# Kernel tuning notes

Measured on AMD Instinct MI355X. Metric: run time of the kernel, lower is better.

## Reference

```python
import jax, jax.numpy as jnp
import numpy as np

B, N, DIM = 16, 3136, 512
HEADS, AGENT, WINDOW = 8, 49, 14


def setup_inputs() -> dict:
    key = jax.random.key(0)
    ks = jax.random.split(key, 14)
    s = 0.02
    return {
        "x": jax.random.normal(ks[0], (B, N, DIM), jnp.float32),
        "w_qkv": jax.random.normal(ks[1], (3 * DIM, DIM), jnp.float32) * 0.02,
        "w_proj": jax.random.normal(ks[2], (DIM, DIM), jnp.float32) * 0.02,
        "b_proj": jnp.zeros((DIM,), jnp.float32),
        "w_dwc": jax.random.normal(ks[3], (DIM, 1, 3, 3), jnp.float32) * 0.1,
        "b_dwc": jnp.zeros((DIM,), jnp.float32),
        "an_bias": jax.random.normal(ks[4], (HEADS, AGENT, 7, 7), jnp.float32) * s,
        "na_bias": jax.random.normal(ks[5], (HEADS, AGENT, 7, 7), jnp.float32) * s,
        "ah_bias": jax.random.normal(ks[6], (1, HEADS, AGENT, WINDOW, 1), jnp.float32) * s,
        "aw_bias": jax.random.normal(ks[7], (1, HEADS, AGENT, 1, WINDOW), jnp.float32) * s,
        "ha_bias": jax.random.normal(ks[8], (1, HEADS, WINDOW, 1, AGENT), jnp.float32) * s,
        "wa_bias": jax.random.normal(ks[9], (1, HEADS, 1, WINDOW, AGENT), jnp.float32) * s,
        "ca_bias": jax.random.normal(ks[10], (1, HEADS, 1, AGENT), jnp.float32) * s,
    }


def reference(x, w_qkv, w_proj, b_proj, w_dwc, b_dwc, an_bias, na_bias,
              ah_bias, aw_bias, ha_bias, wa_bias, ca_bias):
    b, n, c = x.shape
    h = w = int(np.sqrt(n))            # 56x56, static
    nh, hd = HEADS, c // HEADS
    scale = hd ** -0.5
    ww = WINDOW * WINDOW               # 196

    qkv = x @ w_qkv.T                  # (b, n, 3c)
    q, k, v = jnp.split(qkv, 3, axis=-1)

    # agent tokens: adaptive avg-pool q to (7, 7)  (exact block mean, 56/7=8)
    pool = int(AGENT ** 0.5)
    q_img = q.reshape(b, h, w, c).transpose(0, 3, 1, 2)  # (b, c, h, w)
    pooled = q_img.reshape(b, c, pool, h // pool, pool, w // pool).mean(axis=(3, 5))
    agent = pooled.reshape(b, c, AGENT).transpose(0, 2, 1)  # (b, 49, c)

    qh = q.reshape(b, n, nh, hd).transpose(0, 2, 1, 3)      # (b, H, n, d)
    kh = k.reshape(b, n, nh, hd).transpose(0, 2, 1, 3)
    vh = v.reshape(b, n, nh, hd).transpose(0, 2, 1, 3)
    ah = agent.reshape(b, AGENT, nh, hd).transpose(0, 2, 1, 3)  # (b, H, 49, d)

    # ---- stage 1: agent -> kv attention ----
    pb1 = jax.image.resize(an_bias, (nh, AGENT, WINDOW, WINDOW), 'bilinear')
    pb1 = pb1.reshape(1, nh, AGENT, ww)
    pb2 = (ah_bias + aw_bias).reshape(1, nh, AGENT, ww)
    pb = jnp.broadcast_to(pb1 + pb2, (b, nh, AGENT, ww))
    scores1 = jnp.einsum('bhad,bhnd->bhan', ah * scale, kh)     # (b, H, 49, n)
    pb_up = jax.image.resize(pb, scores1.shape, 'bilinear')     # 196 -> n along last dim
    attn1 = jax.nn.softmax(scores1 + pb_up, axis=-1)
    agent_v = jnp.einsum('bhan,bhnd->bhad', attn1, vh)          # (b, H, 49, d)

    # ---- stage 2: query -> agent attention ----
    ab1 = jax.image.resize(na_bias, (nh, AGENT, WINDOW, WINDOW), 'bilinear')
    ab1 = ab1.reshape(1, nh, AGENT, ww).transpose(0, 1, 3, 2)   # (1, H, 196, 49)
    ab2 = (ha_bias + wa_bias).reshape(1, nh, ww, AGENT)
    ab = jnp.broadcast_to(ab1 + ab2, (b, nh, ww, AGENT))
    ab = jnp.concatenate([jnp.broadcast_to(ca_bias, (b, nh, 1, AGENT)), ab], axis=-2)
    scores2 = jnp.einsum('bhnd,bhad->bhna', qh * scale, ah)     # (b, H, n, 49)
    ab_up = jax.image.resize(ab, scores2.shape, 'bilinear')     # 197 -> n along dim -2
    attn2 = jax.nn.softmax(scores2 + ab_up, axis=-1)
    out = jnp.einsum('bhna,bhad->bhnd', attn2, agent_v)
    out = out.transpose(0, 2, 1, 3).reshape(b, n, c)

    # ---- depthwise-conv residual on v ----
    v_img = vh.transpose(0, 2, 1, 3).reshape(b, h, w, c).transpose(0, 3, 1, 2)
    dwc = jax.lax.conv_general_dilated(
        v_img, w_dwc, (1, 1), 'SAME',
        dimension_numbers=('NCHW', 'OIHW', 'NCHW'), feature_group_count=c)
    dwc = dwc + b_dwc[None, :, None, None]
    out = out + dwc.transpose(0, 2, 3, 1).reshape(b, n, c)

    return out @ w_proj.T + b_proj
```

## Files before the change

### kernel.cpp

```cpp
#include <hip/hip_runtime.h>

typedef unsigned short u16;
typedef unsigned int   u32;
typedef unsigned long long u64;
typedef float  f32x4  __attribute__((ext_vector_type(4)));
typedef __bf16 bf16x8 __attribute__((ext_vector_type(8)));

#define DEV static __device__ __forceinline__

DEV float bf2f(u16 u){ union{float f;u32 i;}v; v.i=((u32)u)<<16; return v.f; }
DEV float bflo(u32 u){ union{float f;u32 i;}v; v.i=u<<16; return v.f; }
DEV float bfhi(u32 u){ union{float f;u32 i;}v; v.i=u&0xffff0000u; return v.f; }
DEV u16   f2bf(float f){ union{float f;u32 i;}v; v.f=f; return (u16)((v.i + 0x7fffu + ((v.i>>16)&1u))>>16); }

DEV void async16(const void* g, void* l){
  __builtin_amdgcn_global_load_lds((const __attribute__((address_space(1))) void*)g,
                                   (__attribute__((address_space(3))) void*)l, 16, 0, 0);
}

__global__ __launch_bounds__(256) void cast_bf16(const float* __restrict__ in,
                                                 u16* __restrict__ out, int n4)
{
  int i = blockIdx.x*256 + threadIdx.x;
  if (i >= n4) return;
  float4 v = ((const float4*)in)[i];
  ushort4 o;
  o.x = f2bf(v.x); o.y = f2bf(v.y); o.z = f2bf(v.z); o.w = f2bf(v.w);
  ((ushort4*)out)[i] = o;
}

__global__ __launch_bounds__(256) void gemm_bt(
    const u16* __restrict__ A, const u16* __restrict__ W, int K, int mode,
    u16* __restrict__ oq, u16* __restrict__ okk, u16* __restrict__ ov,
    float* __restrict__ of, const float* __restrict__ bias)
{
  __shared__ __align__(16) u16 As[8192];
  __shared__ __align__(16) u16 Bs[8192];
  const int tid  = threadIdx.x;
  const int wave = tid >> 6, lane = tid & 63;
  const int wm = wave >> 1, wn = wave & 1;
  const int r16 = lane & 15, q4 = lane >> 4;
  const int xr = r16 & 7;
  const size_t Abase = (size_t)blockIdx.x * 128 * K;
  const size_t Bbase = (size_t)blockIdx.y * 128 * K;

  f32x4 acc[4][4];
  #pragma unroll
  for (int i=0;i<4;i++)
    #pragma unroll
    for (int j=0;j<4;j++) acc[i][j] = (f32x4){0.f,0.f,0.f,0.f};

  for (int k0 = 0; k0 < K; k0 += 64) {
    #pragma unroll
    for (int i=0;i<4;i++){
      int s   = i*256 + tid;
      int row = s >> 3;
      int c   = (s & 7) ^ (row & 7);
      async16(A + Abase + (size_t)row*K + k0 + c*8, (char*)As + (size_t)s*16);
      async16(W + Bbase + (size_t)row*K + k0 + c*8, (char*)Bs + (size_t)s*16);
    }
    __syncthreads();
    #pragma unroll
    for (int ks=0; ks<2; ks++){
      const int xo = ((ks*4 + q4) ^ xr) * 8;
      bf16x8 af[4], bfr[4];
      #pragma unroll
      for (int i=0;i<4;i++) af[i]  = *(const bf16x8*)&As[(wm*64 + i*16 + r16)*64 + xo];
      #pragma unroll
      for (int j=0;j<4;j++) bfr[j] = *(const bf16x8*)&Bs[(wn*64 + j*16 + r16)*64 + xo];
      #pragma unroll
      for (int i=0;i<4;i++)
        #pragma unroll
        for (int j=0;j<4;j++)
          acc[i][j] = __builtin_amdgcn_mfma_f32_16x16x32_bf16(bfr[j], af[i], acc[i][j], 0,0,0);
    }
    __syncthreads();
  }

  const int m0 = blockIdx.x*128 + wm*64;
  const int n0 = blockIdx.y*128 + wn*64;
  if (mode == 0){
    int sel = blockIdx.y >> 2;
    u16* dst = sel==0 ? oq : (sel==1 ? okk : ov);
    #pragma unroll
    for (int i=0;i<4;i++){
      int token = m0 + i*16 + r16;
      #pragma unroll
      for (int j=0;j<4;j++){
        int col = (n0 + j*16 + q4*4) & 511;
        uint2 pk;
        pk.x = (u32)f2bf(acc[i][j][0]) | ((u32)f2bf(acc[i][j][1]) << 16);
        pk.y = (u32)f2bf(acc[i][j][2]) | ((u32)f2bf(acc[i][j][3]) << 16);
        *(uint2*)&dst[(size_t)token*512 + col] = pk;
      }
    }
  } else {
    #pragma unroll
    for (int j=0;j<4;j++){
      int nbase = n0 + j*16 + q4*4;
      float4 b4 = *(const float4*)&bias[nbase];
      #pragma unroll
      for (int i=0;i<4;i++){
        int token = m0 + i*16 + r16;
        float4 o4 = { acc[i][j][0]+b4.x, acc[i][j][1]+b4.y,
                      acc[i][j][2]+b4.z, acc[i][j][3]+b4.w };
        *(float4*)&of[(size_t)token*512 + nbase] = o4;
      }
    }
  }
}

__global__ __launch_bounds__(256) void pool_q(const u16* __restrict__ qb, u16* __restrict__ agentb)
{
  int idx = blockIdx.x*256 + threadIdx.x;
  int c = idx & 511;
  int ba = idx >> 9;
  int a = ba & 63, b = ba >> 6;
  if (a >= 49) { agentb[idx] = 0; return; }
  int ay = a / 7, ax = a % 7;
  const u16* base = qb + (size_t)b*3136*512 + c;
  float acc = 0.f;
  #pragma unroll
  for (int iy=0; iy<8; iy++){
    int rowoff = ((ay*8 + iy)*56 + ax*8) * 512;
    #pragma unroll
    for (int ix=0; ix<8; ix++) acc += bf2f(base[(size_t)rowoff + ix*512]);
  }
  agentb[idx] = f2bf(acc * 0.015625f);
}

DEV void lin1(float c, int S, int& i0, int& i1, float& w){
  if (c <= 0.f){ i0=0; i1=0; w=0.f; }
  else if (c >= (float)(S-1)){ i0=S-1; i1=S-1; w=0.f; }
  else { i0=(int)c; i1=i0+1; w=c-(float)i0; }
}
DEV float bilin7(const float* s, int Y, int X){
  int y0,y1,x0,x1; float wy,wx;
  lin1(0.5f*Y - 0.25f, 7, y0,y1,wy);
  lin1(0.5f*X - 0.25f, 7, x0,x1,wx);
  float v0 = s[y0*7+x0] + wx*(s[y0*7+x1]-s[y0*7+x0]);
  float v1 = s[y1*7+x0] + wx*(s[y1*7+x1]-s[y1*7+x0]);
  return v0 + wy*(v1 - v0);
}
__global__ __launch_bounds__(256) void bias_pre(
    const float* __restrict__ an_bias, const float* __restrict__ na_bias,
    const float* __restrict__ ah_bias, const float* __restrict__ aw_bias,
    const float* __restrict__ ha_bias, const float* __restrict__ wa_bias,
    const float* __restrict__ ca_bias, float* __restrict__ PB, float* __restrict__ AB)
{
  int idx = blockIdx.x*256 + threadIdx.x;
  if (idx < 8*49*196){
    int j = idx % 196; int ha = idx / 196; int a = ha % 49, h = ha / 49;
    int wy = j / 14, wx = j % 14;
    PB[idx] = bilin7(an_bias + (h*49+a)*49, wy, wx)
            + ah_bias[(h*49+a)*14 + wy] + aw_bias[(h*49+a)*14 + wx];
  }
  int idx2 = idx - 8*49*196;
  if (idx2 >= 0 && idx2 < 8*197*49){
    int a = idx2 % 49; int hr = idx2 / 49; int r = hr % 197, h = hr / 197;
    float v;
    if (r == 0) v = ca_bias[h*49 + a];
    else {
      int j = r - 1; int wy = j / 14, wx = j % 14;
      v = bilin7(na_bias + (h*49+a)*49, wy, wx)
        + ha_bias[(h*14+wy)*49 + a] + wa_bias[(h*14+wx)*49 + a];
    }
    AB[idx2] = v;
  }
}

__global__ __launch_bounds__(256) void bias_expand2(
    const float* __restrict__ PB, const float* __restrict__ AB,
    float* __restrict__ PBIT, float* __restrict__ ABI)
{
  int idx = blockIdx.x*256 + threadIdx.x;
  if (idx < 1605632) {
    int a = idx & 63; int t = idx >> 6; int n = t % 3136; int h = t / 3136;
    float val = -1e30f;
    if (a < 49) {
      const float* row = PB + (h*49 + a)*196;
      float c1 = (n + 0.5f)*0.0625f - 0.5f;
      if (c1 <= 0.f) val = row[0];
      else if (c1 >= 195.f) val = row[195];
      else { int j0 = (int)c1; float w = c1 - (float)j0; val = row[j0] + w*(row[j0+1]-row[j0]); }
    }
    PBIT[idx] = val;
  } else {
    int idx2 = idx - 1605632;
    if (idx2 >= 1605632) return;
    int a = idx2 & 63; int t = idx2 >> 6; int n = t % 3136; int h = t / 3136;
    float val = -1e30f;
    if (a < 49) {
      float c2 = (n + 0.5f)*(197.0f/3136.0f) - 0.5f;
      int r0; float w;
      if (c2 <= 0.f) { r0 = 0; w = 0.f; }
      else if (c2 >= 196.f) { r0 = 196; w = 0.f; }
      else { r0 = (int)c2; w = c2 - (float)r0; }
      int r1 = (r0 < 196) ? r0 + 1 : 196;
      float v0 = AB[(h*197 + r0)*49 + a];
      float v1 = AB[(h*197 + r1)*49 + a];
      val = v0 + w*(v1 - v0);
    }
    ABI[idx2] = val;
  }
}

__global__ __launch_bounds__(256) void stage1_mfma(
    const u16* __restrict__ kb, const u16* __restrict__ vb,
    const u16* __restrict__ agentb, const float* __restrict__ PBIT,
    float* __restrict__ pav, float* __restrict__ psum)
{
  int bh = blockIdx.x, chunk = blockIdx.y;
  int b = bh >> 3, h = bh & 7;
  int tid = threadIdx.x, lane = tid & 63, w = tid >> 6;
  int r16 = lane & 15, q4 = lane >> 4;
  __shared__ __align__(16) u16 kld[64*64];
  __shared__ __align__(16) u16 vt[64*68];
  __shared__ __align__(16) u16 scb[64*72];

  int agent = w*16 + r16;
  bf16x8 bah[2];
  {
    const u16* ap = agentb + ((size_t)(b*64 + agent))*512 + h*64 + q4*8;
    bah[0] = *(const bf16x8*)ap;
    bah[1] = *(const bf16x8*)(ap + 32);
  }
  f32x4 Oacc[4];
  #pragma unroll
  for (int nt = 0; nt < 4; nt++) Oacc[nt] = (f32x4){0.f,0.f,0.f,0.f};
  float ssum = 0.f;
  int n0 = chunk * 448;
  const u16* kbase = kb + ((size_t)b*3136)*512 + h*64;
  const u16* vbase = vb + ((size_t)b*3136)*512 + h*64;

  for (int it = 0; it < 7; it++) {
    int nt0 = n0 + it*64;
    __syncthreads();
    #pragma unroll
    for (int i = 0; i < 2; i++) {
      int L = w*128 + i*64 + lane;
      int row = L >> 3, colc = (L & 7) ^ (row & 7);
      async16(kbase + (size_t)(nt0 + row)*512 + colc*8, (char*)kld + (w*128 + i*64)*16);
    }
    uint4 va[2]; int vtok[2], vdc[2];
    #pragma unroll
    for (int i = 0; i < 2; i++) {
      int c = tid + i*256;
      vtok[i] = c >> 3; vdc[i] = (c & 7)*8;
      va[i] = *(const uint4*)(vbase + (size_t)(nt0 + vtok[i])*512 + vdc[i]);
    }
    #pragma unroll
    for (int i = 0; i < 2; i++) {
      u32 uu[4] = {va[i].x, va[i].y, va[i].z, va[i].w};
      #pragma unroll
      for (int e = 0; e < 4; e++) {
        vt[(vdc[i] + 2*e + 0)*68 + vtok[i]] = (u16)(uu[e] & 0xffffu);
        vt[(vdc[i] + 2*e + 1)*68 + vtok[i]] = (u16)(uu[e] >> 16);
      }
    }
    __syncthreads();
    f32x4 S[4];
    #pragma unroll
    for (int mt = 0; mt < 4; mt++) S[mt] = (f32x4){0.f,0.f,0.f,0.f};
    #pragma unroll
    for (int ks = 0; ks < 2; ks++)
      #pragma unroll
      for (int mt = 0; mt < 4; mt++) {
        int row = mt*16 + r16;
        int colc = (ks*4 + q4) ^ (row & 7);
        bf16x8 afr = *(const bf16x8*)&kld[row*64 + colc*8];
        S[mt] = __builtin_amdgcn_mfma_f32_16x16x32_bf16(afr, bah[ks], S[mt], 0,0,0);
      }
    #pragma unroll
    for (int mt = 0; mt < 4; mt++) {
      u64 pk = 0;
      #pragma unroll
      for (int r = 0; r < 4; r++) {
        int tokl = mt*16 + q4*4 + r;
        float bias = PBIT[((size_t)h*3136 + nt0 + tokl)*64 + agent];
        float e = __expf(0.125f*S[mt][r] + bias);
        ssum += e;
        pk |= ((u64)f2bf(e)) << (16*r);
      }
      *(u64*)&scb[agent*72 + mt*16 + q4*4] = pk;
    }
    #pragma unroll
    for (int ks = 0; ks < 2; ks++) {
      bf16x8 ap = *(const bf16x8*)&scb[agent*72 + ks*32 + q4*8];
      #pragma unroll
      for (int nt = 0; nt < 4; nt++) {
        union { bf16x8 v; uint2 u[2]; } bb;
        int dim = nt*16 + r16;
        bb.u[0] = *(const uint2*)&vt[dim*68 + ks*32 + q4*8];
        bb.u[1] = *(const uint2*)&vt[dim*68 + ks*32 + q4*8 + 4];
        Oacc[nt] = __builtin_amdgcn_mfma_f32_16x16x32_bf16(ap, bb.v, Oacc[nt], 0,0,0);
      }
    }
  }
  ssum += __shfl_xor(ssum, 16);
  ssum += __shfl_xor(ssum, 32);
  size_t pb = (size_t)chunk*128 + bh;
  #pragma unroll
  for (int nt = 0; nt < 4; nt++)
    #pragma unroll
    for (int r = 0; r < 4; r++)
      pav[(pb*64 + (w*16 + q4*4 + r))*64 + nt*16 + r16] = Oacc[nt][r];
  if (lane < 16) psum[pb*64 + w*16 + lane] = ssum;
}

__global__ __launch_bounds__(256) void reduce_agv(
    const float* __restrict__ pav, const float* __restrict__ psum, u16* __restrict__ avTg)
{
  int idx = blockIdx.x*256 + threadIdx.x;
  int d = idx & 63, a = (idx >> 6) & 63, bh = idx >> 12;
  float val = 0.f;
  if (a < 49) {
    float acc = 0.f, s = 0.f;
    #pragma unroll
    for (int c = 0; c < 7; c++) {
      acc += pav[(((size_t)c*128 + bh)*64 + a)*64 + d];
      s   += psum[((size_t)c*128 + bh)*64 + a];
    }
    val = acc / s;
  }
  avTg[((size_t)bh*64 + d)*72 + a] = f2bf(val);
}

__global__ __launch_bounds__(256) void stage2_mfma(
    const u16* __restrict__ qb, const u16* __restrict__ agentb,
    const u16* __restrict__ avTg, const float* __restrict__ ABI,
    u16* __restrict__ aout)
{
  int bh = blockIdx.x, chunk = blockIdx.y;
  int b = bh >> 3, h = bh & 7;
  int tid = threadIdx.x, lane = tid & 63, w = tid >> 6;
  int r16 = lane & 15, q4 = lane >> 4;
  __shared__ __align__(16) u16 avs[64*72];
  __shared__ __align__(16) u16 scb2[4*16*72];

  const u16* avsrc = avTg + (size_t)bh*4608;
  #pragma unroll
  for (int rr = 0; rr < 3; rr++) {
    int c = rr*256 + w*64 + lane;
    if (c < 576) async16(avsrc + c*8, (char*)avs + ((size_t)rr*256 + w*64)*16);
  }
  bf16x8 bah[4][2];
  #pragma unroll
  for (int nt = 0; nt < 4; nt++) {
    const u16* ap = agentb + ((size_t)(b*64 + nt*16 + r16))*512 + h*64 + q4*8;
    bah[nt][0] = *(const bf16x8*)ap;
    bah[nt][1] = *(const bf16x8*)(ap + 32);
  }
  __syncthreads();

  u16* scw = scb2 + w*16*72;
  for (int t = 0; t < 7; t++) {
    int tok0 = (chunk*28 + w*7 + t)*16;
    bf16x8 aq[2];
    {
      const u16* qp = qb + ((size_t)b*3136 + tok0 + r16)*512 + h*64 + q4*8;
      aq[0] = *(const bf16x8*)qp;
      aq[1] = *(const bf16x8*)(qp + 32);
    }
    f32x4 S[4];
    #pragma unroll
    for (int nt = 0; nt < 4; nt++) S[nt] = (f32x4){0.f,0.f,0.f,0.f};
    #pragma unroll
    for (int ks = 0; ks < 2; ks++)
      #pragma unroll
      for (int nt = 0; nt < 4; nt++)
        S[nt] = __builtin_amdgcn_mfma_f32_16x16x32_bf16(aq[ks], bah[nt][ks], S[nt], 0,0,0);
    float rs[4] = {0.f,0.f,0.f,0.f};
    #pragma unroll
    for (int nt = 0; nt < 4; nt++)
      #pragma unroll
      for (int r = 0; r < 4; r++) {
        int tokl = q4*4 + r;
        float bias = ABI[((size_t)h*3136 + tok0 + tokl)*64 + nt*16 + r16];
        float e = __expf(0.125f*S[nt][r] + bias);
        rs[r] += e;
        scw[tokl*72 + nt*16 + r16] = f2bf(e);
      }
    #pragma unroll
    for (int m = 1; m <= 8; m <<= 1)
      #pragma unroll
      for (int r = 0; r < 4; r++) rs[r] += __shfl_xor(rs[r], m);
    f32x4 O[4];
    #pragma unroll
    for (int nt = 0; nt < 4; nt++) O[nt] = (f32x4){0.f,0.f,0.f,0.f};
    #pragma unroll
    for (int ks = 0; ks < 2; ks++) {
      bf16x8 ap2 = *(const bf16x8*)&scw[r16*72 + ks*32 + q4*8];
      #pragma unroll
      for (int nt = 0; nt < 4; nt++) {
        bf16x8 bv = *(const bf16x8*)&avs[(nt*16 + r16)*72 + ks*32 + q4*8];
        O[nt] = __builtin_amdgcn_mfma_f32_16x16x32_bf16(ap2, bv, O[nt], 0,0,0);
      }
    }
    float inv[4];
    #pragma unroll
    for (int r = 0; r < 4; r++) inv[r] = 1.0f / rs[r];
    #pragma unroll
    for (int nt = 0; nt < 4; nt++)
      #pragma unroll
      for (int r = 0; r < 4; r++)
        aout[((size_t)b*3136 + tok0 + q4*4 + r)*512 + h*64 + nt*16 + r16] = f2bf(O[nt][r]*inv[r]);
  }
}

__global__ __launch_bounds__(256) void dwc_add2(
    const u16* __restrict__ vb, const float* __restrict__ w_dwc,
    const float* __restrict__ b_dwc, u16* __restrict__ io)
{
  int wave = (blockIdx.x << 2) + (threadIdx.x >> 6);
  int lane = threadIdx.x & 63;
  int c0 = lane * 8;

  float wt[9][8];
  {
    float tmp[72];
    const float4* wp = (const float4*)(w_dwc + c0*9);
    #pragma unroll
    for (int i = 0; i < 18; i++) {
      float4 v4 = wp[i];
      tmp[4*i] = v4.x; tmp[4*i+1] = v4.y; tmp[4*i+2] = v4.z; tmp[4*i+3] = v4.w;
    }
    #pragma unroll
    for (int j = 0; j < 8; j++)
      #pragma unroll
      for (int tp = 0; tp < 9; tp++) wt[tp][j] = tmp[j*9 + tp];
  }
  float bias[8];
  {
    const float4* bp = (const float4*)(b_dwc + c0);
    float4 a4 = bp[0], b4 = bp[1];
    bias[0]=a4.x; bias[1]=a4.y; bias[2]=a4.z; bias[3]=a4.w;
    bias[4]=b4.x; bias[5]=b4.y; bias[6]=b4.z; bias[7]=b4.w;
  }

  int t0 = wave * 16;
  int b = t0 / 3136;
  int n0 = t0 - b*3136;
  const u16* vbase = vb + ((size_t)b*3136)*512 + c0;

  for (int ti = 0; ti < 16; ti++) {
    int n = n0 + ti;
    int y = n / 56, x = n - y*56;
    size_t toff = ((size_t)b*3136 + n)*512 + c0;
    float acc[8];
    {
      uint4 uo = *(const uint4*)(io + toff);
      u32 uu[4] = {uo.x, uo.y, uo.z, uo.w};
      #pragma unroll
      for (int e = 0; e < 4; e++) {
        acc[2*e+0] = bflo(uu[e]) + bias[2*e+0];
        acc[2*e+1] = bfhi(uu[e]) + bias[2*e+1];
      }
    }
    #pragma unroll
    for (int dy = 0; dy < 3; dy++) {
      int yy = y + dy - 1;
      if (yy < 0 || yy > 55) continue;
      #pragma unroll
      for (int dx = 0; dx < 3; dx++) {
        int xx = x + dx - 1;
        if (xx < 0 || xx > 55) continue;
        uint4 uv = *(const uint4*)(vbase + ((size_t)(yy*56 + xx) << 9));
        u32 uu[4] = {uv.x, uv.y, uv.z, uv.w};
        const float* wr = wt[dy*3 + dx];
        #pragma unroll
        for (int e = 0; e < 4; e++) {
          acc[2*e+0] += bflo(uu[e]) * wr[2*e+0];
          acc[2*e+1] += bfhi(uu[e]) * wr[2*e+1];
        }
      }
    }
    uint4 pk;
    pk.x = (u32)f2bf(acc[0]) | ((u32)f2bf(acc[1]) << 16);
    pk.y = (u32)f2bf(acc[2]) | ((u32)f2bf(acc[3]) << 16);
    pk.z = (u32)f2bf(acc[4]) | ((u32)f2bf(acc[5]) << 16);
    pk.w = (u32)f2bf(acc[6]) | ((u32)f2bf(acc[7]) << 16);
    *(uint4*)(io + toff) = pk;
  }
}

extern "C" void kernel_launch(void* const* d_in, const int* in_sizes, int n_in,
                              void* d_out, int out_size, void* d_ws, size_t ws_size,
                              hipStream_t stream)
{
  const float* x       = (const float*)d_in[0];
  const float* w_qkv   = (const float*)d_in[1];
  const float* w_proj  = (const float*)d_in[2];
  const float* b_proj  = (const float*)d_in[3];
  const float* w_dwc   = (const float*)d_in[4];
  const float* b_dwc   = (const float*)d_in[5];
  const float* an_bias = (const float*)d_in[6];
  const float* na_bias = (const float*)d_in[7];
  const float* ah_bias = (const float*)d_in[8];
  const float* aw_bias = (const float*)d_in[9];
  const float* ha_bias = (const float*)d_in[10];
  const float* wa_bias = (const float*)d_in[11];
  const float* ca_bias = (const float*)d_in[12];

  if (ws_size < 210000000u) return;

  char* p = (char*)d_ws;
  u16* regA   = (u16*)p;  p += 51380224;
  u16* qb     = (u16*)p;  p += 51380224;
  u16* kb     = (u16*)p;  p += 51380224;
  u16* vb     = (u16*)p;  p += 51380224;
  u16* wqkvb  = (u16*)p;  p += 1572864;
  u16* wprojb = (u16*)p;  p += 524288;
  u16* agentb = (u16*)p;  p += 1048576;
  float* PB   = (float*)p; p += 307456;
  float* AB   = (float*)p; p += 309248;

  float* PBIT = (float*)((char*)regA);
  float* ABI  = (float*)((char*)regA + 6422528);
  float* pav  = (float*)((char*)regA + 12845056);
  float* psum = (float*)((char*)regA + 27525120);
  u16*   avTg = (u16*)  ((char*)regA + 27754496);
  u16*   aout = kb;

  cast_bf16<<<25088, 256, 0, stream>>>(x, regA, 6422528);
  cast_bf16<<<768,   256, 0, stream>>>(w_qkv, wqkvb, 196608);
  cast_bf16<<<256,   256, 0, stream>>>(w_proj, wprojb, 65536);

  gemm_bt<<<dim3(392,12), 256, 0, stream>>>(regA, wqkvb, 512, 0, qb, kb, vb, nullptr, nullptr);
  pool_q<<<2048, 256, 0, stream>>>(qb, agentb);
  bias_pre<<<602, 256, 0, stream>>>(an_bias, na_bias, ah_bias, aw_bias, ha_bias, wa_bias, ca_bias, PB, AB);
  bias_expand2<<<12544, 256, 0, stream>>>(PB, AB, PBIT, ABI);
  stage1_mfma<<<dim3(128,7), 256, 0, stream>>>(kb, vb, agentb, PBIT, pav, psum);
  reduce_agv<<<2048, 256, 0, stream>>>(pav, psum, avTg);
  stage2_mfma<<<dim3(128,7), 256, 0, stream>>>(qb, agentb, avTg, ABI, aout);
  dwc_add2<<<784, 256, 0, stream>>>(vb, w_dwc, b_dwc, aout);
  gemm_bt<<<dim3(392,4), 256, 0, stream>>>(aout, wprojb, 512, 1, nullptr, nullptr, nullptr,
                                           (float*)d_out, b_proj);
}
```

Baseline: 550.3 us.

## Replace 128x128 GEMM with 256x256 double-buffered pipelined MFMA GEMM

Both projection GEMMs now use 256x256 output tiles computed by 512 threads (8 waves) instead of 128x128 tiles with 4 waves, which doubles operand reuse per LDS load. The new kernel double-buffers LDS and issues async global-to-LDS loads for the next K tiles in the middle of the MFMA phases. It coordinates this with explicit barriers, waitcnt instructions and s_setprio, so memory latency can overlap with compute. The catch is 128 KB of LDS per block, more accumulator registers, and fewer blocks in each grid, which can reduce occupancy and load balance across CUs.

Result: faster. 529.6 us (-3.8%).

```diff
diff --git a/kernel.cpp b/kernel.cpp
--- a/kernel.cpp
+++ b/kernel.cpp
@@ -29,65 +29,128 @@
   ((ushort4*)out)[i] = o;
 }
 
-__global__ __launch_bounds__(256) void gemm_bt(
+__global__ __launch_bounds__(512, 2) void gemm256(
     const u16* __restrict__ A, const u16* __restrict__ W, int K, int mode,
     u16* __restrict__ oq, u16* __restrict__ okk, u16* __restrict__ ov,
     float* __restrict__ of, const float* __restrict__ bias)
 {
-  __shared__ __align__(16) u16 As[8192];
-  __shared__ __align__(16) u16 Bs[8192];
+  __shared__ __align__(16) u16 As[2*16384];
+  __shared__ __align__(16) u16 Bs[2*16384];
   const int tid  = threadIdx.x;
-  const int wave = tid >> 6, lane = tid & 63;
-  const int wm = wave >> 1, wn = wave & 1;
+  const int w = tid >> 6, lane = tid & 63;
+  const int wm = w >> 2, wn = w & 3;
   const int r16 = lane & 15, q4 = lane >> 4;
   const int xr = r16 & 7;
-  const size_t Abase = (size_t)blockIdx.x * 128 * K;
-  const size_t Bbase = (size_t)blockIdx.y * 128 * K;
-
-  f32x4 acc[4][4];
+  const size_t Abase = (size_t)blockIdx.x * 256 * K;
+  const size_t Bbase = (size_t)blockIdx.y * 256 * K;
+  const int NT = K >> 6;
+
+#define STAGE(t, half, arr) do { \
+    const u16* _src = (arr) ? (W + Bbase) : (A + Abase); \
+    u16* _dst = ((arr) ? Bs : As) + (((t) & 1) * 16384 + (half) * 8192); \
+    const int _k0 = (t) << 6; \
+    _Pragma("unroll") \
+    for (int _i = 0; _i < 2; _i++) { \
+      int _s = _i*512 + tid; \
+      int _row = _s >> 3; \
+      int _c = (_s & 7) ^ (_row & 7); \
+      async16(_src + (size_t)((half)*128 + _row) * K + _k0 + _c*8, (char*)_dst + (size_t)_s * 16); \
+    } \
+  } while(0)
+
+#define READ_A(MI0) do { \
+    _Pragma("unroll") \
+    for (int _i = 0; _i < 4; _i++) { \
+      int _row = wm*128 + ((MI0)+_i)*16 + r16; \
+      _Pragma("unroll") \
+      for (int _ks = 0; _ks < 2; _ks++) \
+        af[_i][_ks] = *(const bf16x8*)&As[boff + _row*64 + (((_ks*4 + q4) ^ xr) * 8)]; \
+    } \
+  } while(0)
+
+#define READ_B() do { \
+    _Pragma("unroll") \
+    for (int _j = 0; _j < 4; _j++) { \
+      int _row = wn*64 + _j*16 + r16; \
+      _Pragma("unroll") \
+      for (int _ks = 0; _ks < 2; _ks++) \
+        bfr[_j][_ks] = *(const bf16x8*)&Bs[boff + _row*64 + (((_ks*4 + q4) ^ xr) * 8)]; \
+    } \
+  } while(0)
+
+#define MFMA_Q(MI0, NI0) do { \
+    _Pragma("unroll") \
+    for (int _ks = 0; _ks < 2; _ks++) \
+      _Pragma("unroll") \
+      for (int _i = 0; _i < 4; _i++) \
+        _Pragma("unroll") \
+        for (int _j = 0; _j < 2; _j++) \
+          acc[(MI0)+_i][(NI0)+_j] = __builtin_amdgcn_mfma_f32_16x16x32_bf16( \
+              bfr[(NI0)+_j][_ks], af[_i][_ks], acc[(MI0)+_i][(NI0)+_j], 0,0,0); \
+  } while(0)
+
+  f32x4 acc[8][4];
   #pragma unroll
-  for (int i=0;i<4;i++)
+  for (int i=0;i<8;i++)
     #pragma unroll
     for (int j=0;j<4;j++) acc[i][j] = (f32x4){0.f,0.f,0.f,0.f};
-
-  for (int k0 = 0; k0 < K; k0 += 64) {
-    #pragma unroll
-    for (int i=0;i<4;i++){
-      int s   = i*256 + tid;
-      int row = s >> 3;
-      int c   = (s & 7) ^ (row & 7);
-      async16(A + Abase + (size_t)row*K + k0 + c*8, (char*)As + (size_t)s*16);
-      async16(W + Bbase + (size_t)row*K + k0 + c*8, (char*)Bs + (size_t)s*16);
-    }
-    __syncthreads();
-    #pragma unroll
-    for (int ks=0; ks<2; ks++){
-      const int xo = ((ks*4 + q4) ^ xr) * 8;
-      bf16x8 af[4], bfr[4];
-      #pragma unroll
-      for (int i=0;i<4;i++) af[i]  = *(const bf16x8*)&As[(wm*64 + i*16 + r16)*64 + xo];
-      #pragma unroll
-      for (int j=0;j<4;j++) bfr[j] = *(const bf16x8*)&Bs[(wn*64 + j*16 + r16)*64 + xo];
-      #pragma unroll
-      for (int i=0;i<4;i++)
-        #pragma unroll
-        for (int j=0;j<4;j++)
-          acc[i][j] = __builtin_amdgcn_mfma_f32_16x16x32_bf16(bfr[j], af[i], acc[i][j], 0,0,0);
-    }
-    __syncthreads();
-  }
-
-  const int m0 = blockIdx.x*128 + wm*64;
-  const int n0 = blockIdx.y*128 + wn*64;
+  bf16x8 af[4][2], bfr[4][2];
+
+  STAGE(0,0,0); STAGE(0,1,0); STAGE(0,0,1); STAGE(0,1,1);
+  STAGE(1,0,1); STAGE(1,0,0); STAGE(1,1,0);
+  asm volatile("s_waitcnt vmcnt(6)" ::: "memory");
+  __builtin_amdgcn_s_barrier();
+
+  for (int T = 0; T < NT; ++T) {
+    const int boff = (T & 1) * 16384;
+    READ_A(0);
+    READ_B();
+    if (T+1 < NT) STAGE(T+1, 1, 1);
+    __builtin_amdgcn_s_barrier();
+    asm volatile("s_waitcnt lgkmcnt(0)" ::: "memory");
+    __builtin_amdgcn_sched_barrier(0);
+    __builtin_amdgcn_s_setprio(1);
+    MFMA_Q(0, 0);
+    __builtin_amdgcn_s_setprio(0);
+    __builtin_amdgcn_s_barrier();
+    __builtin_amdgcn_s_setprio(1);
+    MFMA_Q(0, 2);
+    __builtin_amdgcn_s_setprio(0);
+    __builtin_amdgcn_s_barrier();
+    READ_A(4);
+    if (T+2 < NT) STAGE(T+2, 0, 1);
+    __builtin_amdgcn_s_barrier();
+    asm volatile("s_waitcnt lgkmcnt(0)" ::: "memory");
+    __builtin_amdgcn_sched_barrier(0);
+    __builtin_amdgcn_s_setprio(1);
+    MFMA_Q(4, 0);
+    __builtin_amdgcn_s_setprio(0);
+    __builtin_amdgcn_s_barrier();
+    if (T+2 < NT) { STAGE(T+2, 0, 0); STAGE(T+2, 1, 0); }
+    __builtin_amdgcn_s_setprio(1);
+    MFMA_Q(4, 2);
+    __builtin_amdgcn_s_setprio(0);
+    if (T+2 < NT)      asm volatile("s_waitcnt vmcnt(6)" ::: "memory");
+    else if (T+1 < NT) asm volatile("s_waitcnt vmcnt(0)" ::: "memory");
+    __builtin_amdgcn_s_barrier();
+  }
+
+#undef STAGE
+#undef READ_A
+#undef READ_B
+#undef MFMA_Q
+
+  const int m0  = blockIdx.x*256 + wm*128;
+  const int n0g = blockIdx.y*256 + wn*64;
   if (mode == 0){
-    int sel = blockIdx.y >> 2;
+    int sel = blockIdx.y >> 1;
     u16* dst = sel==0 ? oq : (sel==1 ? okk : ov);
     #pragma unroll
-    for (int i=0;i<4;i++){
+    for (int i=0;i<8;i++){
       int token = m0 + i*16 + r16;
       #pragma unroll
       for (int j=0;j<4;j++){
-        int col = (n0 + j*16 + q4*4) & 511;
+        int col = (n0g + j*16 + q4*4) & 511;
         uint2 pk;
         pk.x = (u32)f2bf(acc[i][j][0]) | ((u32)f2bf(acc[i][j][1]) << 16);
         pk.y = (u32)f2bf(acc[i][j][2]) | ((u32)f2bf(acc[i][j][3]) << 16);
@@ -97,10 +160,10 @@
   } else {
     #pragma unroll
     for (int j=0;j<4;j++){
-      int nbase = n0 + j*16 + q4*4;
+      int nbase = n0g + j*16 + q4*4;
       float4 b4 = *(const float4*)&bias[nbase];
       #pragma unroll
-      for (int i=0;i<4;i++){
+      for (int i=0;i<8;i++){
         int token = m0 + i*16 + r16;
         float4 o4 = { acc[i][j][0]+b4.x, acc[i][j][1]+b4.y,
                       acc[i][j][2]+b4.z, acc[i][j][3]+b4.w };
@@ -526,7 +589,7 @@
   cast_bf16<<<768,   256, 0, stream>>>(w_qkv, wqkvb, 196608);
   cast_bf16<<<256,   256, 0, stream>>>(w_proj, wprojb, 65536);
 
-  gemm_bt<<<dim3(392,12), 256, 0, stream>>>(regA, wqkvb, 512, 0, qb, kb, vb, nullptr, nullptr);
+  gemm256<<<dim3(196,6), 512, 0, stream>>>(regA, wqkvb, 512, 0, qb, kb, vb, nullptr, nullptr);
   pool_q<<<2048, 256, 0, stream>>>(qb, agentb);
   bias_pre<<<602, 256, 0, stream>>>(an_bias, na_bias, ah_bias, aw_bias, ha_bias, wa_bias, ca_bias, PB, AB);
   bias_expand2<<<12544, 256, 0, stream>>>(PB, AB, PBIT, ABI);
@@ -534,6 +597,6 @@
   reduce_agv<<<2048, 256, 0, stream>>>(pav, psum, avTg);
   stage2_mfma<<<dim3(128,7), 256, 0, stream>>>(qb, agentb, avTg, ABI, aout);
   dwc_add2<<<784, 256, 0, stream>>>(vb, w_dwc, b_dwc, aout);
-  gemm_bt<<<dim3(392,4), 256, 0, stream>>>(aout, wprojb, 512, 1, nullptr, nullptr, nullptr,
+  gemm256<<<dim3(196,2), 512, 0, stream>>>(aout, wprojb, 512, 1, nullptr, nullptr, nullptr,
                                            (float*)d_out, b_proj);
 }
```
